# Performance work log

Hardware: AMD Instinct MI355X
Metric: run time of the kernel (lower is better)

## Reference

```python
import jax, jax.numpy as jnp
import numpy as np

B, T, D, S, K = 4, 4096, 1024, 2048, 8

def _l2norm(v, axis=-1, eps=1e-12):
    # matches torch F.normalize: v / max(||v||, eps)
    n = jnp.sqrt(jnp.sum(v * v, axis=axis, keepdims=True))
    return v / jnp.maximum(n, eps)

def setup_inputs() -> dict:
    key = jax.random.key(0)
    ks = jax.random.split(key, 9)
    H = D // 2
    return {
        "x": jax.random.normal(ks[0], (B, T, D), dtype=jnp.float32),
        "memory_keys": jax.random.normal(ks[1], (S, D), dtype=jnp.float32) * 0.02,
        "memory_values": jax.random.normal(ks[2], (S, D), dtype=jnp.float32) * 0.02,
        "Wq": jax.random.normal(ks[3], (D, D), dtype=jnp.float32) * (1.0 / np.sqrt(D)),
        "Wo": jax.random.normal(ks[4], (D, D), dtype=jnp.float32) * (1.0 / np.sqrt(D)),
        "gW1": jax.random.normal(ks[5], (H, 2 * D), dtype=jnp.float32) * (1.0 / np.sqrt(2 * D)),
        "gb1": jnp.zeros((H,), dtype=jnp.float32),
        "gW2": jax.random.normal(ks[6], (1, H), dtype=jnp.float32) * (1.0 / np.sqrt(H)),
        "gb2": jnp.zeros((1,), dtype=jnp.float32),
    }

def reference(x, memory_keys, memory_values, Wq, Wo, gW1, gb1, gW2, gb2):
    # query projection (Linear, no bias): y = x @ W.T
    queries = jnp.einsum('btd,ed->bte', x, Wq)
    keys_norm = _l2norm(memory_keys)          # [S, D]
    queries_norm = _l2norm(queries)           # [B, T, D]
    # cosine similarities [B, T, S]
    sims = jnp.einsum('btd,sd->bts', queries_norm, keys_norm)
    topk_sims, topk_idx = jax.lax.top_k(sims, K)      # [B, T, K]
    topk_w = jax.nn.softmax(topk_sims, axis=-1)       # [B, T, K]
    topk_vals = memory_values[topk_idx]               # [B, T, K, D]
    retrieved = jnp.einsum('btk,btkd->btd', topk_w, topk_vals)
    retrieved = jnp.einsum('btd,ed->bte', retrieved, Wo)
    gate_in = jnp.concatenate([x, retrieved], axis=-1)           # [B, T, 2D]
    h = jax.nn.gelu(jnp.einsum('btc,hc->bth', gate_in, gW1) + gb1, approximate=False)
    gate = jax.nn.sigmoid(jnp.einsum('bth,oh->bto', h, gW2) + gb2)  # [B, T, 1]
    return x + gate * retrieved
```

## Files before the change

kernel.cpp:

```cpp
#include <hip/hip_runtime.h>
#include <math.h>

#define NROWS 16384
#define DDIM  1024
#define SKEYS 2048
#define KTOP  8
#define HDIM  512

typedef short  s16x8 __attribute__((ext_vector_type(8)));
typedef float  f32x4 __attribute__((ext_vector_type(4)));

#define GL16(g, l) __builtin_amdgcn_global_load_lds(                      \
    (const __attribute__((address_space(1))) void*)(g),                   \
    (__attribute__((address_space(3))) void*)(l), 16, 0, 0)

__device__ __forceinline__ float wave_sum(float v) {
#pragma unroll
    for (int off = 32; off > 0; off >>= 1) v += __shfl_xor(v, off, 64);
    return v;
}

__device__ __forceinline__ unsigned short f2bf(float f) {
    union { float f; unsigned u; } c; c.f = f;
    unsigned u = c.u;
    unsigned r = (u + 0x7FFFu + ((u >> 16) & 1u)) >> 16;
    return (unsigned short)r;
}

__device__ __forceinline__ float gelu_exact(float v) {
    return 0.5f * v * (1.0f + erff(v * 0.7071067811865475f));
}

__device__ __forceinline__ ushort4 cvt4(float4 v) {
    ushort4 o;
    o.x = f2bf(v.x); o.y = f2bf(v.y); o.z = f2bf(v.z); o.w = f2bf(v.w);
    return o;
}

__global__ __launch_bounds__(256) void prep_kernel(
        const float* __restrict__ x,   const float* __restrict__ Wq,
        const float* __restrict__ Wo,  const float* __restrict__ mv,
        const float* __restrict__ gW1, const float* __restrict__ mk,
        unsigned short* __restrict__ x_bf, unsigned short* __restrict__ wqcat,
        unsigned short* __restrict__ wo_bf, unsigned short* __restrict__ mv_bf,
        unsigned short* __restrict__ gw1b, unsigned short* __restrict__ kn) {
    int bid = blockIdx.x, t = threadIdx.x;
    {
        float4 v = ((const float4*)(mk + (size_t)bid * DDIM))[t];
        float ss = v.x * v.x + v.y * v.y + v.z * v.z + v.w * v.w;
        ss = wave_sum(ss);
        __shared__ float wsum[4];
        if ((t & 63) == 0) wsum[t >> 6] = ss;
        __syncthreads();
        float tot = wsum[0] + wsum[1] + wsum[2] + wsum[3];
        float sc = 1.0f / fmaxf(sqrtf(tot), 1e-12f);
        float4 o = make_float4(v.x * sc, v.y * sc, v.z * sc, v.w * sc);
        ((ushort4*)(kn + (size_t)bid * DDIM))[t] = cvt4(o);
    }
    int gid = bid * 256 + t, stride = gridDim.x * 256;
    for (int i = gid; i < NROWS * DDIM / 4; i += stride)
        ((ushort4*)x_bf)[i] = cvt4(((const float4*)x)[i]);
    for (int i = gid; i < DDIM * DDIM / 4; i += stride)
        ((ushort4*)wqcat)[i] = cvt4(((const float4*)Wq)[i]);
    for (int i = gid; i < HDIM * 2 * DDIM / 4; i += stride) {
        float4 v = ((const float4*)gW1)[i];
        int r = i >> 9, c4 = i & 511;
        if (c4 < 256) ((ushort4*)wqcat)[DDIM * DDIM / 4 + r * 256 + c4] = cvt4(v);
        else          ((ushort4*)gw1b)[r * 256 + (c4 - 256)] = cvt4(v);
    }
    for (int i = gid; i < DDIM * DDIM / 4; i += stride)
        ((ushort4*)wo_bf)[i] = cvt4(((const float4*)Wo)[i]);
    for (int i = gid; i < SKEYS * DDIM / 4; i += stride)
        ((ushort4*)mv_bf)[i] = cvt4(((const float4*)mv)[i]);
}

struct GArg {
    const unsigned short* A;
    const unsigned short* B;
    unsigned short* C;
    unsigned short* C2;
    float* qinv;
    int Ncols, N2cols, nsplit, gx, nblocks, mode;
};

__global__ __launch_bounds__(256, 3) void dualgemm(GArg g0, GArg g1, int split) {
    __shared__ __align__(16) unsigned short As[2][4096];
    __shared__ __align__(16) unsigned short Bs[2][4096];

    int tid = threadIdx.x, l = tid & 63, wid = tid >> 6;
    bool first = ((int)blockIdx.x < split);
    GArg g = first ? g0 : g1;
    int bid = first ? blockIdx.x : blockIdx.x - split;
    int cpx = g.nblocks >> 3;
    int sbid = (bid & 7) * cpx + (bid >> 3);
    int m0 = (sbid / g.gx) * 128;
    int n0 = (sbid % g.gx) * 128;

    int wr = wid >> 1, wc = wid & 1;
    constexpr int NT = 32;

    f32x4 acc[4][4];
#pragma unroll
    for (int i = 0; i < 4; ++i)
#pragma unroll
        for (int j = 0; j < 4; ++j) acc[i][j] = (f32x4){0.f, 0.f, 0.f, 0.f};

    int srow   = tid >> 2;
    int schunk = (tid & 3) ^ ((srow >> 1) & 3);
    int offA[2], offB[2];
#pragma unroll
    for (int i = 0; i < 2; ++i) {
        offA[i] = (m0 + i * 64 + srow) * 1024;
        offB[i] = (n0 + i * 64 + srow) * 1024;
    }
    int ldsU = wid * 512;

#define STAGE(bsel, kt_)                                                       \
    do {                                                                       \
        int gk_ = (kt_) * 32 + schunk * 8;                                     \
        _Pragma("unroll")                                                      \
        for (int i_ = 0; i_ < 2; ++i_) {                                       \
            GL16(g.A + offA[i_] + gk_, &As[bsel][i_ * 2048 + ldsU]);           \
            GL16(g.B + offB[i_] + gk_, &Bs[bsel][i_ * 2048 + ldsU]);           \
        }                                                                      \
    } while (0)

    STAGE(0, 0);

    int frow = l & 15;
    int fp   = (l >> 4) ^ ((frow >> 1) & 3);
    int aoff = (wr * 64 + frow) * 32 + fp * 8;
    int boff = (wc * 64 + frow) * 32 + fp * 8;

#pragma unroll 2
    for (int kt = 0; kt < NT; ++kt) {
        int b = kt & 1;
        if (kt + 1 < NT) {
            STAGE(b ^ 1, kt + 1);
            asm volatile("s_waitcnt vmcnt(4)" ::: "memory");
        } else {
            asm volatile("s_waitcnt vmcnt(0)" ::: "memory");
        }
        __builtin_amdgcn_s_barrier();
        asm volatile("" ::: "memory");

        s16x8 af[4], bfr[4];
#pragma unroll
        for (int mf = 0; mf < 4; ++mf)
            af[mf] = *(const s16x8*)&As[b][aoff + mf * 512];
#pragma unroll
        for (int nf = 0; nf < 4; ++nf)
            bfr[nf] = *(const s16x8*)&Bs[b][boff + nf * 512];

        __builtin_amdgcn_s_setprio(1);
#pragma unroll
        for (int mf = 0; mf < 4; ++mf)
#pragma unroll
            for (int nf = 0; nf < 4; ++nf)
                acc[mf][nf] = __builtin_amdgcn_mfma_f32_16x16x32_bf16(
                    af[mf], bfr[nf], acc[mf][nf], 0, 0, 0);
        __builtin_amdgcn_s_setprio(0);
        asm volatile("" ::: "memory");
        __builtin_amdgcn_s_barrier();
        asm volatile("" ::: "memory");
    }
#undef STAGE

    unsigned short* cptr = g.C;
    int nc = g.Ncols, cb = n0;
    bool qreg = (g.mode == 2);
    if (g.mode == 2 && n0 >= g.nsplit) {
        cptr = g.C2; nc = g.N2cols; cb = n0 - g.nsplit; qreg = false;
    }

    int crow = (l >> 4) << 2;
    int ccol = l & 15;
    float rs[4][4];
#pragma unroll
    for (int i = 0; i < 4; ++i)
#pragma unroll
        for (int j = 0; j < 4; ++j) rs[i][j] = 0.f;

#pragma unroll
    for (int mf = 0; mf < 4; ++mf) {
        int gr = m0 + wr * 64 + mf * 16 + crow;
#pragma unroll
        for (int nf = 0; nf < 4; ++nf) {
            int gc = cb + wc * 64 + nf * 16 + ccol;
            f32x4 v = acc[mf][nf];
#pragma unroll
            for (int r2 = 0; r2 < 4; ++r2) {
                float o = v[r2];
                unsigned short sv = f2bf(o);
                if (g.mode == 3)
                    sv = sv ^ ((sv & 0x8000) ? 0xFFFFu : 0x8000u);
                cptr[(size_t)(gr + r2) * nc + gc] = sv;
                if (qreg) rs[mf][r2] += o * o;
            }
        }
    }
    if (qreg) {
#pragma unroll
        for (int mf = 0; mf < 4; ++mf)
#pragma unroll
            for (int r2 = 0; r2 < 4; ++r2) {
                float s = rs[mf][r2];
                s += __shfl_xor(s, 1, 64);
                s += __shfl_xor(s, 2, 64);
                s += __shfl_xor(s, 4, 64);
                s += __shfl_xor(s, 8, 64);
                if ((l & 15) == 0)
                    atomicAdd(&g.qinv[m0 + wr * 64 + mf * 16 + (l >> 4) * 4 + r2], s);
            }
    }
}

#define BINS(arr, xk)                                                     \
    do {                                                                  \
        unsigned cur_ = (xk);                                             \
        _Pragma("unroll")                                                 \
        for (int p_ = 0; p_ < 8; ++p_) {                                  \
            unsigned mx_ = arr[p_] > cur_ ? arr[p_] : cur_;               \
            unsigned mn_ = arr[p_] > cur_ ? cur_ : arr[p_];               \
            arr[p_] = mx_; cur_ = mn_;                                    \
        }                                                                 \
    } while (0)

__global__ __launch_bounds__(256) void mega_kernel(
        const float* __restrict__ qsum,
        const unsigned short* __restrict__ sims,
        const unsigned short* __restrict__ x_bf,
        const unsigned short* __restrict__ xg1,
        const unsigned short* __restrict__ mvo,
        const unsigned short* __restrict__ mvog,
        const float* __restrict__ gb1, const float* __restrict__ gW2,
        const float* __restrict__ gb2, float* __restrict__ out) {
    int wid = threadIdx.x >> 6, l = threadIdx.x & 63;
    int row = blockIdx.x * 4 + wid;

    float qs = 1.0f / fmaxf(sqrtf(qsum[row]), 1e-12f);

    const unsigned short* sr = sims + (size_t)row * SKEYS;
    unsigned a[8], bb[8];
#pragma unroll
    for (int j = 0; j < 8; ++j) { a[j] = 0u; bb[j] = 0u; }
#pragma unroll
    for (int c = 0; c < 4; ++c) {
        uint4 raw = *(const uint4*)(sr + c * 512 + l * 8);
        unsigned wv[4] = {raw.x, raw.y, raw.z, raw.w};
#pragma unroll
        for (int q2 = 0; q2 < 4; ++q2) {
            unsigned bi0 = (unsigned)(c * 512 + l * 8 + q2 * 2);
            unsigned klo = ((wv[q2] & 0xFFFFu) << 16) | bi0;
            unsigned khi = (wv[q2] & 0xFFFF0000u) | (bi0 + 1);
            if (c < 2) { BINS(a, klo); BINS(a, khi); }
            else       { BINS(bb, klo); BINS(bb, khi); }
        }
    }
#pragma unroll
    for (int j = 0; j < 8; ++j) BINS(a, bb[j]);

    float ov[8]; int oi[8];
#pragma unroll
    for (int j = 0; j < 8; ++j) {
        unsigned best = a[0];
#pragma unroll
        for (int off = 32; off > 0; off >>= 1) {
            unsigned o2 = (unsigned)__shfl_xor((int)best, off, 64);
            best = best > o2 ? best : o2;
        }
        oi[j] = (int)(best & 0xFFFFu);
        unsigned short ks = (unsigned short)(best >> 16);
        unsigned short sv = ks ^ ((ks & 0x8000) ? 0x8000u : 0xFFFFu);
        ov[j] = __uint_as_float(((unsigned)sv) << 16);
        bool hit = (a[0] == best);
#pragma unroll
        for (int p = 0; p < 7; ++p) a[p] = hit ? a[p + 1] : a[p];
        a[7] = hit ? 0u : a[7];
    }

    float w[KTOP];
    float m = ov[0] * qs, ssum = 0.f;
#pragma unroll
    for (int j = 0; j < 8; ++j) { w[j] = expf(ov[j] * qs - m); ssum += w[j]; }
    float sinv = 1.0f / ssum;
#pragma unroll
    for (int j = 0; j < 8; ++j) w[j] *= sinv;

    float r2[16], hp[8];
#pragma unroll
    for (int j = 0; j < 16; ++j) r2[j] = 0.f;
#pragma unroll
    for (int j = 0; j < 8; ++j) hp[j] = 0.f;
#pragma unroll
    for (int k = 0; k < KTOP; ++k) {
        float wk = w[k];
        const unsigned short* mo = mvo + (size_t)oi[k] * DDIM + l * 16;
        uint4 a0 = *(const uint4*)mo;
        uint4 a1 = *(const uint4*)(mo + 8);
        const unsigned short* mg = mvog + (size_t)oi[k] * HDIM + l * 8;
        uint4 g0 = *(const uint4*)mg;
        unsigned aw[8] = {a0.x, a0.y, a0.z, a0.w, a1.x, a1.y, a1.z, a1.w};
#pragma unroll
        for (int j = 0; j < 8; ++j) {
            r2[2 * j]     += wk * __uint_as_float(aw[j] << 16);
            r2[2 * j + 1] += wk * __uint_as_float(aw[j] & 0xffff0000u);
        }
        unsigned gw[4] = {g0.x, g0.y, g0.z, g0.w};
#pragma unroll
        for (int j = 0; j < 4; ++j) {
            hp[2 * j]     += wk * __uint_as_float(gw[j] << 16);
            hp[2 * j + 1] += wk * __uint_as_float(gw[j] & 0xffff0000u);
        }
    }
    uint4 xg = *(const uint4*)(xg1 + (size_t)row * HDIM + l * 8);
    unsigned xgw[4] = {xg.x, xg.y, xg.z, xg.w};
    float p = 0.f;
#pragma unroll
    for (int j = 0; j < 4; ++j) {
        float h0 = gelu_exact(hp[2 * j] + __uint_as_float(xgw[j] << 16)
                              + gb1[l * 8 + 2 * j]);
        float h1 = gelu_exact(hp[2 * j + 1] + __uint_as_float(xgw[j] & 0xffff0000u)
                              + gb1[l * 8 + 2 * j + 1]);
        p += h0 * gW2[l * 8 + 2 * j] + h1 * gW2[l * 8 + 2 * j + 1];
    }
    p = wave_sum(p);
    float gate = 1.0f / (1.0f + expf(-(p + gb2[0])));
    const unsigned short* xr = x_bf + (size_t)row * DDIM + l * 16;
    uint4 x0 = *(const uint4*)xr, x1 = *(const uint4*)(xr + 8);
    unsigned xw[8] = {x0.x, x0.y, x0.z, x0.w, x1.x, x1.y, x1.z, x1.w};
    float o[16];
#pragma unroll
    for (int j = 0; j < 8; ++j) {
        o[2 * j]     = __uint_as_float(xw[j] << 16)         + gate * r2[2 * j];
        o[2 * j + 1] = __uint_as_float(xw[j] & 0xffff0000u) + gate * r2[2 * j + 1];
    }
    float4* po = (float4*)(out + (size_t)row * DDIM + l * 16);
    po[0] = make_float4(o[0], o[1], o[2], o[3]);
    po[1] = make_float4(o[4], o[5], o[6], o[7]);
    po[2] = make_float4(o[8], o[9], o[10], o[11]);
    po[3] = make_float4(o[12], o[13], o[14], o[15]);
}

extern "C" void kernel_launch(void* const* d_in, const int* in_sizes, int n_in,
                              void* d_out, int out_size, void* d_ws, size_t ws_size,
                              hipStream_t stream) {
    (void)in_sizes; (void)n_in; (void)out_size; (void)ws_size;
    const float* x   = (const float*)d_in[0];
    const float* mk  = (const float*)d_in[1];
    const float* mv  = (const float*)d_in[2];
    const float* Wq  = (const float*)d_in[3];
    const float* Wo  = (const float*)d_in[4];
    const float* gW1 = (const float*)d_in[5];
    const float* gb1 = (const float*)d_in[6];
    const float* gW2 = (const float*)d_in[7];
    const float* gb2 = (const float*)d_in[8];
    float* out = (float*)d_out;

    char* w = (char*)d_ws;
    unsigned short* x_bf    = (unsigned short*)w;  w += (size_t)NROWS * DDIM * 2;
    unsigned short* q_bf    = (unsigned short*)w;  w += (size_t)NROWS * DDIM * 2;
    unsigned short* xg1_bf  = (unsigned short*)w;  w += (size_t)NROWS * HDIM * 2;
    unsigned short* kn_bf   = (unsigned short*)w;  w += (size_t)SKEYS * DDIM * 2;
    unsigned short* wqcat   = (unsigned short*)w;  w += (size_t)(DDIM + HDIM) * DDIM * 2;
    unsigned short* gw1b_bf = (unsigned short*)w;  w += (size_t)HDIM * DDIM * 2;
    unsigned short* wo_bf   = (unsigned short*)w;  w += (size_t)DDIM * DDIM * 2;
    unsigned short* mv_bf   = (unsigned short*)w;  w += (size_t)SKEYS * DDIM * 2;
    unsigned short* mvo_bf  = (unsigned short*)w;  w += (size_t)SKEYS * DDIM * 2;
    unsigned short* mvog_bf = (unsigned short*)w;  w += (size_t)SKEYS * HDIM * 2;
    unsigned short* sims    = (unsigned short*)w;  w += (size_t)NROWS * SKEYS * 2;
    float* qsum = (float*)w;                       w += (size_t)NROWS * 4;

    hipMemsetAsync(qsum, 0, (size_t)NROWS * sizeof(float), stream);

    prep_kernel<<<SKEYS, 256, 0, stream>>>(x, Wq, Wo, mv, gW1, mk,
                                           x_bf, wqcat, wo_bf, mv_bf, gw1b_bf, kn_bf);

    {
        GArg gq; gq.A = x_bf;  gq.B = wqcat; gq.C = q_bf;  gq.C2 = xg1_bf;
        gq.qinv = qsum; gq.Ncols = DDIM; gq.N2cols = HDIM; gq.nsplit = DDIM;
        gq.gx = 12; gq.nblocks = 1536; gq.mode = 2;
        GArg gm; gm.A = mv_bf; gm.B = wo_bf; gm.C = mvo_bf; gm.C2 = nullptr;
        gm.qinv = nullptr; gm.Ncols = DDIM; gm.N2cols = 0; gm.nsplit = 0;
        gm.gx = 8; gm.nblocks = 128; gm.mode = 0;
        dualgemm<<<1664, 256, 0, stream>>>(gq, gm, 1536);
    }

    {
        GArg gs; gs.A = q_bf;   gs.B = kn_bf;   gs.C = sims;    gs.C2 = nullptr;
        gs.qinv = nullptr; gs.Ncols = SKEYS; gs.N2cols = 0; gs.nsplit = 0;
        gs.gx = 16; gs.nblocks = 2048; gs.mode = 3;
        GArg gg; gg.A = mvo_bf; gg.B = gw1b_bf; gg.C = mvog_bf; gg.C2 = nullptr;
        gg.qinv = nullptr; gg.Ncols = HDIM; gg.N2cols = 0; gg.nsplit = 0;
        gg.gx = 4; gg.nblocks = 64; gg.mode = 0;
        dualgemm<<<2112, 256, 0, stream>>>(gs, gg, 2048);
    }

    mega_kernel<<<NROWS / 4, 256, 0, stream>>>(
        qsum, sims, x_bf, xg1_bf, mvo_bf, mvog_bf, gb1, gW2, gb2, out);
}
```

Before: 286.3 us.

## Replace top-k insertion with bitonic sort-merge and drop atomic norm accumulation

The per-lane top-8 selection moves from repeated insertion into running lists to bitonic sorting networks over 32 keys, followed by a butterfly merge across the wave. This replaces eight serial rounds of shuffle-max-and-pop. Query squared-norm partials are now written to 16 separate slots instead of atomically added, which removes the memset and the atomic traffic. Loads of x, xg1 and the norm partials are issued early in the fused kernel to overlap with the sort. The cost is a larger register footprint for the 32 keys and 16 extra partial reads per row.

```diff
diff --git a/kernel.cpp b/kernel.cpp
--- a/kernel.cpp
+++ b/kernel.cpp
@@ -79,7 +79,7 @@
     const unsigned short* B;
     unsigned short* C;
     unsigned short* C2;
-    float* qinv;
+    float* qpart;
     int Ncols, N2cols, nsplit, gx, nblocks, mode;
 };
 
@@ -200,6 +200,7 @@
         }
     }
     if (qreg) {
+        int slot = (n0 >> 7) * 2 + wc;
 #pragma unroll
         for (int mf = 0; mf < 4; ++mf)
 #pragma unroll
@@ -210,24 +211,43 @@
                 s += __shfl_xor(s, 4, 64);
                 s += __shfl_xor(s, 8, 64);
                 if ((l & 15) == 0)
-                    atomicAdd(&g.qinv[m0 + wr * 64 + mf * 16 + (l >> 4) * 4 + r2], s);
+                    g.qpart[(size_t)slot * NROWS +
+                            (m0 + wr * 64 + mf * 16 + (l >> 4) * 4 + r2)] = s;
             }
     }
 }
 
-#define BINS(arr, xk)                                                     \
-    do {                                                                  \
-        unsigned cur_ = (xk);                                             \
-        _Pragma("unroll")                                                 \
-        for (int p_ = 0; p_ < 8; ++p_) {                                  \
-            unsigned mx_ = arr[p_] > cur_ ? arr[p_] : cur_;               \
-            unsigned mn_ = arr[p_] > cur_ ? cur_ : arr[p_];               \
-            arr[p_] = mx_; cur_ = mn_;                                    \
-        }                                                                 \
-    } while (0)
+#define CED(k, i, j)                                                      \
+    { unsigned mx_ = k[i] > k[j] ? k[i] : k[j];                           \
+      unsigned mn_ = k[i] > k[j] ? k[j] : k[i];                           \
+      k[i] = mx_; k[j] = mn_; }
+
+__device__ __forceinline__ void sort8d(unsigned* k) {
+    CED(k,0,1) CED(k,2,3) CED(k,4,5) CED(k,6,7)
+    CED(k,0,2) CED(k,1,3) CED(k,4,6) CED(k,5,7)
+    CED(k,1,2) CED(k,5,6)
+    CED(k,0,4) CED(k,1,5) CED(k,2,6) CED(k,3,7)
+    CED(k,2,4) CED(k,3,5)
+    CED(k,1,2) CED(k,3,4) CED(k,5,6)
+}
+
+__device__ __forceinline__ void bclean8d(unsigned* t) {
+    CED(t,0,4) CED(t,1,5) CED(t,2,6) CED(t,3,7)
+    CED(t,0,2) CED(t,1,3) CED(t,4,6) CED(t,5,7)
+    CED(t,0,1) CED(t,2,3) CED(t,4,5) CED(t,6,7)
+}
+
+__device__ __forceinline__ void merge8d(unsigned* a, const unsigned* b) {
+    unsigned t[8];
+#pragma unroll
+    for (int i = 0; i < 8; ++i) t[i] = a[i] > b[7 - i] ? a[i] : b[7 - i];
+    bclean8d(t);
+#pragma unroll
+    for (int i = 0; i < 8; ++i) a[i] = t[i];
+}
 
 __global__ __launch_bounds__(256) void mega_kernel(
-        const float* __restrict__ qsum,
+        const float* __restrict__ qpart,
         const unsigned short* __restrict__ sims,
         const unsigned short* __restrict__ x_bf,
         const unsigned short* __restrict__ xg1,
@@ -238,47 +258,63 @@
     int wid = threadIdx.x >> 6, l = threadIdx.x & 63;
     int row = blockIdx.x * 4 + wid;
 
-    float qs = 1.0f / fmaxf(sqrtf(qsum[row]), 1e-12f);
-
     const unsigned short* sr = sims + (size_t)row * SKEYS;
-    unsigned a[8], bb[8];
-#pragma unroll
-    for (int j = 0; j < 8; ++j) { a[j] = 0u; bb[j] = 0u; }
-#pragma unroll
-    for (int c = 0; c < 4; ++c) {
-        uint4 raw = *(const uint4*)(sr + c * 512 + l * 8);
-        unsigned wv[4] = {raw.x, raw.y, raw.z, raw.w};
-#pragma unroll
-        for (int q2 = 0; q2 < 4; ++q2) {
-            unsigned bi0 = (unsigned)(c * 512 + l * 8 + q2 * 2);
-            unsigned klo = ((wv[q2] & 0xFFFFu) << 16) | bi0;
-            unsigned khi = (wv[q2] & 0xFFFF0000u) | (bi0 + 1);
-            if (c < 2) { BINS(a, klo); BINS(a, khi); }
-            else       { BINS(bb, klo); BINS(bb, khi); }
-        }
-    }
-#pragma unroll
-    for (int j = 0; j < 8; ++j) BINS(a, bb[j]);
+    uint4 raw0 = *(const uint4*)(sr + 0 * 512 + l * 8);
+    uint4 raw1 = *(const uint4*)(sr + 1 * 512 + l * 8);
+    uint4 raw2 = *(const uint4*)(sr + 2 * 512 + l * 8);
+    uint4 raw3 = *(const uint4*)(sr + 3 * 512 + l * 8);
+    const unsigned short* xr = x_bf + (size_t)row * DDIM + l * 16;
+    uint4 x0 = *(const uint4*)xr, x1 = *(const uint4*)(xr + 8);
+    uint4 xg = *(const uint4*)(xg1 + (size_t)row * HDIM + l * 8);
+
+    float ssq = 0.f;
+#pragma unroll
+    for (int j = 0; j < 16; ++j) ssq += qpart[(size_t)j * NROWS + row];
+    float qs = 1.0f / fmaxf(sqrtf(ssq), 1e-12f);
+
+    unsigned key[32];
+    {
+        unsigned rw[16] = {raw0.x, raw0.y, raw0.z, raw0.w,
+                           raw1.x, raw1.y, raw1.z, raw1.w,
+                           raw2.x, raw2.y, raw2.z, raw2.w,
+                           raw3.x, raw3.y, raw3.z, raw3.w};
+#pragma unroll
+        for (int c = 0; c < 4; ++c)
+#pragma unroll
+            for (int q2 = 0; q2 < 4; ++q2) {
+                unsigned v = rw[c * 4 + q2];
+                unsigned bi0 = (unsigned)(c * 512 + l * 8 + q2 * 2);
+                key[c * 8 + q2 * 2]     = ((v & 0xFFFFu) << 16) | bi0;
+                key[c * 8 + q2 * 2 + 1] = (v & 0xFFFF0000u) | (bi0 + 1);
+            }
+    }
+    sort8d(key); sort8d(key + 8); sort8d(key + 16); sort8d(key + 24);
+    merge8d(key, key + 8);
+    merge8d(key + 16, key + 24);
+    merge8d(key, key + 16);
+
+#pragma unroll
+    for (int off = 1; off <= 32; off <<= 1) {
+        unsigned br[8];
+#pragma unroll
+        for (int i = 0; i < 8; ++i)
+            br[i] = (unsigned)__shfl_xor((int)key[7 - i], off, 64);
+        unsigned t[8];
+#pragma unroll
+        for (int i = 0; i < 8; ++i) t[i] = key[i] > br[i] ? key[i] : br[i];
+        bclean8d(t);
+#pragma unroll
+        for (int i = 0; i < 8; ++i) key[i] = t[i];
+    }
 
     float ov[8]; int oi[8];
 #pragma unroll
     for (int j = 0; j < 8; ++j) {
-        unsigned best = a[0];
-#pragma unroll
-        for (int off = 32; off > 0; off >>= 1) {
-            unsigned o2 = (unsigned)__shfl_xor((int)best, off, 64);
-            best = best > o2 ? best : o2;
-        }
-        oi[j] = (int)(best & 0xFFFFu);
-        unsigned short ks = (unsigned short)(best >> 16);
+        oi[j] = (int)(key[j] & 0xFFFFu);
+        unsigned short ks = (unsigned short)(key[j] >> 16);
         unsigned short sv = ks ^ ((ks & 0x8000) ? 0x8000u : 0xFFFFu);
         ov[j] = __uint_as_float(((unsigned)sv) << 16);
-        bool hit = (a[0] == best);
-#pragma unroll
-        for (int p = 0; p < 7; ++p) a[p] = hit ? a[p + 1] : a[p];
-        a[7] = hit ? 0u : a[7];
-    }
-
+    }
     float w[KTOP];
     float m = ov[0] * qs, ssum = 0.f;
 #pragma unroll
@@ -313,7 +349,6 @@
             hp[2 * j + 1] += wk * __uint_as_float(gw[j] & 0xffff0000u);
         }
     }
-    uint4 xg = *(const uint4*)(xg1 + (size_t)row * HDIM + l * 8);
     unsigned xgw[4] = {xg.x, xg.y, xg.z, xg.w};
     float p = 0.f;
 #pragma unroll
@@ -326,8 +361,6 @@
     }
     p = wave_sum(p);
     float gate = 1.0f / (1.0f + expf(-(p + gb2[0])));
-    const unsigned short* xr = x_bf + (size_t)row * DDIM + l * 16;
-    uint4 x0 = *(const uint4*)xr, x1 = *(const uint4*)(xr + 8);
     unsigned xw[8] = {x0.x, x0.y, x0.z, x0.w, x1.x, x1.y, x1.z, x1.w};
     float o[16];
 #pragma unroll
@@ -369,33 +402,31 @@
     unsigned short* mvo_bf  = (unsigned short*)w;  w += (size_t)SKEYS * DDIM * 2;
     unsigned short* mvog_bf = (unsigned short*)w;  w += (size_t)SKEYS * HDIM * 2;
     unsigned short* sims    = (unsigned short*)w;  w += (size_t)NROWS * SKEYS * 2;
-    float* qsum = (float*)w;                       w += (size_t)NROWS * 4;
-
-    hipMemsetAsync(qsum, 0, (size_t)NROWS * sizeof(float), stream);
+    float* qpart = (float*)w;                      w += (size_t)16 * NROWS * 4;
 
     prep_kernel<<<SKEYS, 256, 0, stream>>>(x, Wq, Wo, mv, gW1, mk,
                                            x_bf, wqcat, wo_bf, mv_bf, gw1b_bf, kn_bf);
 
     {
         GArg gq; gq.A = x_bf;  gq.B = wqcat; gq.C = q_bf;  gq.C2 = xg1_bf;
-        gq.qinv = qsum; gq.Ncols = DDIM; gq.N2cols = HDIM; gq.nsplit = DDIM;
+        gq.qpart = qpart; gq.Ncols = DDIM; gq.N2cols = HDIM; gq.nsplit = DDIM;
         gq.gx = 12; gq.nblocks = 1536; gq.mode = 2;
         GArg gm; gm.A = mv_bf; gm.B = wo_bf; gm.C = mvo_bf; gm.C2 = nullptr;
-        gm.qinv = nullptr; gm.Ncols = DDIM; gm.N2cols = 0; gm.nsplit = 0;
+        gm.qpart = nullptr; gm.Ncols = DDIM; gm.N2cols = 0; gm.nsplit = 0;
         gm.gx = 8; gm.nblocks = 128; gm.mode = 0;
         dualgemm<<<1664, 256, 0, stream>>>(gq, gm, 1536);
     }
 
     {
         GArg gs; gs.A = q_bf;   gs.B = kn_bf;   gs.C = sims;    gs.C2 = nullptr;
-        gs.qinv = nullptr; gs.Ncols = SKEYS; gs.N2cols = 0; gs.nsplit = 0;
+        gs.qpart = nullptr; gs.Ncols = SKEYS; gs.N2cols = 0; gs.nsplit = 0;
         gs.gx = 16; gs.nblocks = 2048; gs.mode = 3;
         GArg gg; gg.A = mvo_bf; gg.B = gw1b_bf; gg.C = mvog_bf; gg.C2 = nullptr;
-        gg.qinv = nullptr; gg.Ncols = HDIM; gg.N2cols = 0; gg.nsplit = 0;
+        gg.qpart = nullptr; gg.Ncols = HDIM; gg.N2cols = 0; gg.nsplit = 0;
         gg.gx = 4; gg.nblocks = 64; gg.mode = 0;
         dualgemm<<<2112, 256, 0, stream>>>(gs, gg, 2048);
     }
 
     mega_kernel<<<NROWS / 4, 256, 0, stream>>>(
-        qsum, sims, x_bf, xg1_bf, mvo_bf, mvog_bf, gb1, gW2, gb2, out);
-}
+        qpart, sims, x_bf, xg1_bf, mvo_bf, mvog_bf, gb1, gW2, gb2, out);
+}
```

After: 264.3 us. 7.7% less time.
